# Optimization experiments

Measured on AMD Instinct MI355X. Metric: run time of the kernel, lower is better.

## Reference

```python
import jax, jax.numpy as jnp
import numpy as np
jax.config.update("jax_enable_x64", True)  # hashing uses int64 primes as in torch

N_PTS = 1048576
L, T, F = 16, 2 ** 18, 2
N_MIN, N_MAX = 16, 1024
HID, OUT = 64, 3


def setup_inputs() -> dict:
    key = jax.random.key(0)
    ks = jax.random.split(key, 6)
    X = jax.random.uniform(ks[0], (N_PTS, 2), dtype=jnp.float32)
    hash_table = jax.random.uniform(ks[1], (L, T, F), dtype=jnp.float32,
                                    minval=-1e-4, maxval=1e-4)
    def lin(k, fan_in, fan_out):
        bound = 1.0 / np.sqrt(fan_in)
        kw, kb = jax.random.split(k)
        W = jax.random.uniform(kw, (fan_in, fan_out), dtype=jnp.float32,
                               minval=-bound, maxval=bound)
        b = jax.random.uniform(kb, (fan_out,), dtype=jnp.float32,
                               minval=-bound, maxval=bound)
        return W, b
    W1, b1 = lin(ks[2], L * F, HID)
    W2, b2 = lin(ks[3], HID, HID)
    W3, b3 = lin(ks[4], HID, HID)
    W4, b4 = lin(ks[5], HID, OUT)
    return {"X": X, "hash_table": hash_table,
            "W1": W1, "b1": b1, "W2": W2, "b2": b2,
            "W3": W3, "b3": b3, "W4": W4, "b4": b4}


def reference(X, hash_table, W1, b1, W2, b2, W3, b3, W4, b4):
    Lh, Th, Fh = hash_table.shape
    # per-level resolutions: floor(N_min * b**l), b geometric between N_min and N_max
    b_geo = np.exp((np.log(N_MAX) - np.log(N_MIN)) / (Lh - 1))
    N_values = jnp.floor(jnp.asarray(N_MIN * b_geo ** np.arange(Lh),
                                     dtype=jnp.float32))  # (L,)

    x_scaled = X[:, :, None] * N_values[None, None, :]        # (N, 2, L)
    x_floor = jnp.floor(x_scaled)

    # NOTE: original code MULTIPLIES floor coords by the 0/1 vertex pattern
    # (not add) -- we replicate that math faithfully.
    vertices = jnp.array([[0., 0., 1., 1.], [0., 1., 0., 1.]],
                         dtype=jnp.float32)                   # (2, 4)
    x_vert = (x_floor[:, :, :, None] * vertices[None, :, None, :]
              ).astype(jnp.int64)                             # (N, 2, L, 4)

    primes = jnp.array([1, 2654435761], dtype=jnp.int64)
    hv = x_vert * primes[None, :, None, None]
    x_hash = jnp.remainder(jnp.bitwise_xor(hv[:, 0], hv[:, 1]), Th)  # (N, L, 4)

    # irregular gather: per-level hash table lookup -> (N, L, 4, F)
    lookup = hash_table[jnp.arange(Lh)[None, :, None], x_hash]

    w = x_scaled - x_floor                                    # (N, 2, L)
    fx, fy = w[:, 0, :], w[:, 1, :]
    cx, cy = 1.0 - fx, 1.0 - fy
    f_stack = jnp.stack([cx * cy, cx * fy, fx * cy, fx * fy], axis=2)  # (N, L, 4)

    x_interp = jnp.sum(f_stack[:, :, :, None] * lookup, axis=2)  # (N, L, F)
    feat = x_interp.reshape(-1, Lh * Fh).astype(jnp.float32)     # (N, 32)

    h = jax.nn.leaky_relu(feat @ W1 + b1)
    h = jax.nn.leaky_relu(h @ W2 + b2)
    h = jax.nn.leaky_relu(h @ W3 + b3)
    return jax.nn.relu(h @ W4 + b4)
```

## Files before the change

### kernel.cpp

```cpp
#include <hip/hip_runtime.h>
#include <math.h>

typedef _Float16 half8  __attribute__((ext_vector_type(8)));
typedef float    float4v __attribute__((ext_vector_type(4)));

constexpr int T_ = 1 << 18;
constexpr unsigned TMASK = T_ - 1;
constexpr unsigned PRIME = 2654435761u;

constexpr int WFRAG_HALFS = 22 * 64 * 8;
constexpr int BIAS_FLOATS = 208;
constexpr int WS_BYTES    = 22528 + 240 * 4;
constexpr int WS_UINT4    = WS_BYTES / 16;
constexpr int V12_OFF     = 23488;
constexpr int V3T_OFF     = 57344;
constexpr size_t V3T_BYTES = (size_t)16 * T_ * 4;

constexpr int BLK   = 256;
constexpr int PTS_PER_BLOCK = 512;

struct Meta { float n[16]; float off[16]; };

__global__ void prep_weights(const float* __restrict__ W1, const float* __restrict__ b1,
                             const float* __restrict__ W2, const float* __restrict__ b2,
                             const float* __restrict__ W3, const float* __restrict__ b3,
                             const float* __restrict__ W4, const float* __restrict__ b4,
                             const float2* __restrict__ table,
                             _Float16* __restrict__ wsW, float* __restrict__ wsB,
                             uint2* __restrict__ wsV, Meta mv)
{
    const int tid = threadIdx.x;
    const int bid = blockIdx.x;
    if (bid < 44) {
        const int e = bid * 256 + tid;
        const int frag = e >> 9;
        const int l    = (e >> 3) & 63;
        const int j    = e & 7;
        const int g = l >> 4, m = l & 15;
        const int u = j >> 2, r = j & 3;
        float v;
        if (frag < 4) {
            v = W1[(8*g + j) * 64 + 16*frag + m];
        } else if (frag < 12) {
            const int s = (frag - 4) >> 2, t = (frag - 4) & 3;
            v = W2[(32*s + 16*u + 4*g + r) * 64 + 16*t + m];
        } else if (frag < 20) {
            const int s = (frag - 12) >> 2, t = (frag - 12) & 3;
            v = W3[(32*s + 16*u + 4*g + r) * 64 + 16*t + m];
        } else {
            const int s = frag - 20;
            v = (m < 3) ? W4[(32*s + 16*u + 4*g + r) * 3 + m] : 0.f;
        }
        wsW[e] = (_Float16)v;
    } else if (bid == 44) {
        if (tid < 64) { wsB[tid] = b1[tid]; wsB[64 + tid] = b2[tid]; wsB[128 + tid] = b3[tid]; }
        else if (tid < 80)  { const int r2 = tid - 64; wsB[192 + r2] = (r2 < 3) ? b4[r2] : 0.f; }
        else if (tid < 96)  wsB[BIAS_FLOATS + (tid - 80)] = mv.n[tid - 80];
        else if (tid < 112) wsB[BIAS_FLOATS + 16 + (tid - 96)] = mv.off[tid - 96];
    } else {
        const int e = (bid - 45) * 256 + tid;
        const int total = (int)mv.off[15] + (int)mv.n[15] + 1;
        if (e < total) {
            int l = 0;
            #pragma unroll
            for (int k = 1; k < 16; ++k) if (e >= (int)mv.off[k]) l = k;
            const int i = e - (int)mv.off[l];
            const float2* tl = table + (size_t)l * T_;
            const float2 b = tl[((unsigned)i * PRIME) & TMASK];
            const float2 a = tl[i];
            union { _Float16 h[2]; unsigned u; } p0, p1;
            p0.h[0] = (_Float16)b.x; p0.h[1] = (_Float16)b.y;
            p1.h[0] = (_Float16)a.x; p1.h[1] = (_Float16)a.y;
            wsV[e] = uint2{p0.u, p1.u};
        }
    }
}

__global__ void prep_table_f16(const float2* __restrict__ table, unsigned* __restrict__ t16)
{
    const size_t i = (size_t)blockIdx.x * 256 + threadIdx.x;
    const float2 v = table[i];
    union { _Float16 h[2]; unsigned u; } p;
    p.h[0] = (_Float16)v.x; p.h[1] = (_Float16)v.y;
    t16[i] = p.u;
}

struct Gather {
    float2   v3f[4];
    unsigned v3u[4];
    unsigned v1[4];
    unsigned v2[4];
};

template<bool F16T>
__device__ __forceinline__ void issue_gather(Gather& G, const float2 xy,
                                             const float2* __restrict__ table,
                                             const unsigned* __restrict__ t16,
                                             const unsigned* __restrict__ gV12,
                                             const float (&nvq)[4], const int (&offq)[4],
                                             const int g)
{
    #pragma unroll
    for (int q = 0; q < 4; ++q) {
        const float n = nvq[q];
        const float xs = xy.x * n, ys = xy.y * n;
        const int xi = (int)floorf(xs);
        const int yi = (int)floorf(ys);
        const unsigned yp = (unsigned)yi * PRIME;
        const size_t idx = (size_t)(4*g + q) * T_ + (((unsigned)xi ^ yp) & TMASK);
        if constexpr (F16T) G.v3u[q] = t16[idx];
        else                G.v3f[q] = table[idx];
        G.v1[q] = gV12[2*(offq[q] + yi) + 0];
        G.v2[q] = gV12[2*(offq[q] + xi) + 1];
    }
}

template<bool F16T>
__device__ __forceinline__ half8 make_feat(const float2 xy, const Gather& G,
                                           const float (&nvq)[4],
                                           const float2 (&v0c)[4])
{
    half8 feat;
    #pragma unroll
    for (int q = 0; q < 4; ++q) {
        const float n = nvq[q];
        const float xs = xy.x * n, ys = xy.y * n;
        const float xf = floorf(xs), yf = floorf(ys);
        const float fx = xs - xf, fy = ys - yf;
        union { unsigned u; _Float16 h[2]; } u1, u2, u3;
        u1.u = G.v1[q]; u2.u = G.v2[q];
        float v3x, v3y;
        if constexpr (F16T) { u3.u = G.v3u[q]; v3x = (float)u3.h[0]; v3y = (float)u3.h[1]; }
        else                { v3x = G.v3f[q].x; v3y = G.v3f[q].y; }
        const float cx = 1.f - fx, cy = 1.f - fy;
        const float w0 = cx*cy, w1 = cx*fy, w2 = fx*cy, w3 = fx*fy;
        feat[2*q+0] = (_Float16)(w0*v0c[q].x + w1*(float)u1.h[0] + w2*(float)u2.h[0] + w3*v3x);
        feat[2*q+1] = (_Float16)(w0*v0c[q].y + w1*(float)u1.h[1] + w2*(float)u2.h[1] + w3*v3y);
    }
    return feat;
}

__device__ __forceinline__ void repack(const float4v (&acc)[4], half8& a0, half8& a1)
{
    #pragma unroll
    for (int u = 0; u < 2; ++u)
        #pragma unroll
        for (int r = 0; r < 4; ++r) {
            const float v0 = acc[u][r];
            const float v1 = acc[2 + u][r];
            a0[4*u + r] = (_Float16)(v0 > 0.f ? v0 : 0.01f * v0);
            a1[4*u + r] = (_Float16)(v1 > 0.f ? v1 : 0.01f * v1);
        }
}

template<bool F16T>
__global__ __launch_bounds__(BLK)
void fused_hashnerf_mfma(const float2* __restrict__ X,
                         const float2* __restrict__ table,
                         const uint4* __restrict__ ws,
                         float* __restrict__ out)
{
    __shared__ uint4 sRaw[WS_UINT4];

    const int tid = threadIdx.x;
    for (int i = tid; i < WS_UINT4; i += BLK) sRaw[i] = ws[i];
    __syncthreads();

    const _Float16* Wl = (const _Float16*)sRaw;
    const float*    Bl = (const float*)(sRaw + (22528 / 16));
    const unsigned* gV12 = (const unsigned*)((const char*)ws + V12_OFF);
    const unsigned* t16  = (const unsigned*)((const char*)ws + V3T_OFF);

    const int wave = tid >> 6, lane = tid & 63;
    const int g = lane >> 4, c = lane & 15;

    float4v b1f[4], b2f[4], b3f[4], b4f;
    #pragma unroll
    for (int t = 0; t < 4; ++t) {
        b1f[t] = *(const float4v*)(Bl +       16*t + 4*g);
        b2f[t] = *(const float4v*)(Bl +  64 + 16*t + 4*g);
        b3f[t] = *(const float4v*)(Bl + 128 + 16*t + 4*g);
    }
    b4f = *(const float4v*)(Bl + 192 + 4*g);
    float nvq[4];
    int   offq[4];
    #pragma unroll
    for (int q = 0; q < 4; ++q) {
        nvq[q]  = Bl[BIAS_FLOATS + 4*g + q];
        offq[q] = (int)Bl[BIAS_FLOATS + 16 + 4*g + q];
    }

    const int base_pt = blockIdx.x * PTS_PER_BLOCK + wave * 128;

    float2 xy[8];
    #pragma unroll
    for (int it = 0; it < 8; ++it) xy[it] = X[base_pt + it*16 + c];

    float2 v0c[4];
    #pragma unroll
    for (int q = 0; q < 4; ++q) v0c[q] = table[(size_t)(4*g + q) * T_];

    Gather G0, G1, G2;
    issue_gather<F16T>(G0, xy[0], table, t16, gV12, nvq, offq, g);
    issue_gather<F16T>(G1, xy[1], table, t16, gV12, nvq, offq, g);

    #pragma unroll
    for (int it = 0; it < 8; ++it) {
        Gather& Gc = (it % 3 == 0) ? G0 : (it % 3 == 1) ? G1 : G2;
        Gather& Gn = ((it + 2) % 3 == 0) ? G0 : ((it + 2) % 3 == 1) ? G1 : G2;

        const half8 feat = make_feat<F16T>(xy[it], Gc, nvq, v0c);

        if (it < 6) issue_gather<F16T>(Gn, xy[it+2], table, t16, gV12, nvq, offq, g);
        __builtin_amdgcn_sched_barrier(0);

        float4v acc[4];
        #pragma unroll
        for (int t = 0; t < 4; ++t) {
            const half8 wf = *(const half8*)(Wl + (t*64 + lane)*8);
            acc[t] = __builtin_amdgcn_mfma_f32_16x16x32_f16(wf, feat, b1f[t], 0, 0, 0);
        }

        half8 a0, a1;
        repack(acc, a0, a1);
        #pragma unroll
        for (int t = 0; t < 4; ++t) {
            const half8 w0f = *(const half8*)(Wl + ((4 + t)*64 + lane)*8);
            const half8 w1f = *(const half8*)(Wl + ((8 + t)*64 + lane)*8);
            float4v a = __builtin_amdgcn_mfma_f32_16x16x32_f16(w0f, a0, b2f[t], 0, 0, 0);
            acc[t]    = __builtin_amdgcn_mfma_f32_16x16x32_f16(w1f, a1, a,      0, 0, 0);
        }

        repack(acc, a0, a1);
        #pragma unroll
        for (int t = 0; t < 4; ++t) {
            const half8 w0f = *(const half8*)(Wl + ((12 + t)*64 + lane)*8);
            const half8 w1f = *(const half8*)(Wl + ((16 + t)*64 + lane)*8);
            float4v a = __builtin_amdgcn_mfma_f32_16x16x32_f16(w0f, a0, b3f[t], 0, 0, 0);
            acc[t]    = __builtin_amdgcn_mfma_f32_16x16x32_f16(w1f, a1, a,      0, 0, 0);
        }

        repack(acc, a0, a1);
        const half8 w40 = *(const half8*)(Wl + (20*64 + lane)*8);
        const half8 w41 = *(const half8*)(Wl + (21*64 + lane)*8);
        float4v o = __builtin_amdgcn_mfma_f32_16x16x32_f16(w40, a0, b4f, 0, 0, 0);
        o         = __builtin_amdgcn_mfma_f32_16x16x32_f16(w41, a1, o,   0, 0, 0);
        if (g == 0) {
            float* op = out + (size_t)3 * (base_pt + it * 16 + c);
            op[0] = fmaxf(o[0], 0.f);
            op[1] = fmaxf(o[1], 0.f);
            op[2] = fmaxf(o[2], 0.f);
        }
    }
}

extern "C" void kernel_launch(void* const* d_in, const int* in_sizes, int n_in,
                              void* d_out, int out_size, void* d_ws, size_t ws_size,
                              hipStream_t stream) {
    const float2* X     = (const float2*)d_in[0];
    const float2* table = (const float2*)d_in[1];
    const float*  W1    = (const float*)d_in[2];
    const float*  b1    = (const float*)d_in[3];
    const float*  W2    = (const float*)d_in[4];
    const float*  b2    = (const float*)d_in[5];
    const float*  W3    = (const float*)d_in[6];
    const float*  b3    = (const float*)d_in[7];
    const float*  W4    = (const float*)d_in[8];
    const float*  b4    = (const float*)d_in[9];
    float* out          = (float*)d_out;

    const int npts = in_sizes[0] / 2;

    Meta mv;
    const double bg = exp((log(1024.0) - log(16.0)) / 15.0);
    int acc = 0;
    for (int l = 0; l < 16; ++l) {
        const float nl = floorf((float)(16.0 * pow(bg, (double)l)));
        mv.n[l]   = nl;
        mv.off[l] = (float)acc;
        acc += (int)nl + 1;
    }

    _Float16* wsW = (_Float16*)d_ws;
    float*    wsB = (float*)((char*)d_ws + 22528);
    uint2*    wsV = (uint2*)((char*)d_ws + V12_OFF);
    unsigned* t16 = (unsigned*)((char*)d_ws + V3T_OFF);

    const bool f16t = ws_size >= (size_t)V3T_OFF + V3T_BYTES;

    prep_weights<<<62, 256, 0, stream>>>(W1, b1, W2, b2, W3, b3, W4, b4, table,
                                         wsW, wsB, wsV, mv);
    if (f16t) {
        prep_table_f16<<<16 * T_ / 256, 256, 0, stream>>>(table, t16);
        fused_hashnerf_mfma<true><<<npts / PTS_PER_BLOCK, BLK, 0, stream>>>(
            X, table, (const uint4*)d_ws, out);
    } else {
        fused_hashnerf_mfma<false><<<npts / PTS_PER_BLOCK, BLK, 0, stream>>>(
            X, table, (const uint4*)d_ws, out);
    }
}
```

Measured before the change: 213.4 us.

## Spatially bucket-sort input points before fused hash-grid MLP kernel

Adds a counting sort of input points into a 256x256 spatial grid (histogram, single-block scan, atomic scatter), then runs the fused kernel on the sorted points and writes outputs through the inverse permutation. The aim is better cache locality for the random hash-table gathers, since nearby points hit similar table entries. The cost is three extra kernels plus a memset and a large atomic histogram on every call. Output writes also become scattered, and the sorted path only runs when the workspace is large enough.

Measured after the change: 311.0 us. +45.8%, slower.

```diff
diff --git a/kernel.cpp b/kernel.cpp
--- a/kernel.cpp
+++ b/kernel.cpp
@@ -15,6 +15,8 @@
 constexpr int V12_OFF     = 23488;
 constexpr int V3T_OFF     = 57344;
 constexpr size_t V3T_BYTES = (size_t)16 * T_ * 4;
+constexpr size_t XS_OFF    = (size_t)V3T_OFF + V3T_BYTES;
+constexpr int NBUCK = 256 * 256;
 
 constexpr int BLK   = 256;
 constexpr int PTS_PER_BLOCK = 512;
@@ -85,6 +87,52 @@
     t16[i] = p.u;
 }
 
+__device__ __forceinline__ int bucket_key(const float2 p) {
+    int kx = (int)(p.x * 256.f); kx = kx > 255 ? 255 : kx;
+    int ky = (int)(p.y * 256.f); ky = ky > 255 ? 255 : ky;
+    return (ky << 8) | kx;
+}
+
+__global__ void s_hist(const float2* __restrict__ X, unsigned* __restrict__ hist, int npts)
+{
+    const int i = blockIdx.x * 256 + threadIdx.x;
+    if (i < npts) atomicAdd(&hist[bucket_key(X[i])], 1u);
+}
+
+__global__ __launch_bounds__(1024) void s_scan(unsigned* __restrict__ hist)
+{
+    __shared__ unsigned part[1024];
+    const int t = threadIdx.x;
+    unsigned sum = 0;
+    for (int k = 0; k < 64; ++k) sum += hist[t * 64 + k];
+    part[t] = sum;
+    __syncthreads();
+    for (int d = 1; d < 1024; d <<= 1) {
+        const unsigned v = (t >= d) ? part[t - d] : 0u;
+        __syncthreads();
+        part[t] += v;
+        __syncthreads();
+    }
+    unsigned run = (t == 0) ? 0u : part[t - 1];
+    for (int k = 0; k < 64; ++k) {
+        const unsigned c = hist[t * 64 + k];
+        hist[t * 64 + k] = run;
+        run += c;
+    }
+}
+
+__global__ void s_scatter(const float2* __restrict__ X, unsigned* __restrict__ off,
+                          float2* __restrict__ Xs, unsigned* __restrict__ idx, int npts)
+{
+    const int i = blockIdx.x * 256 + threadIdx.x;
+    if (i < npts) {
+        const float2 p = X[i];
+        const unsigned d = atomicAdd(&off[bucket_key(p)], 1u);
+        Xs[d] = p;
+        idx[d] = (unsigned)i;
+    }
+}
+
 struct Gather {
     float2   v3f[4];
     unsigned v3u[4];
@@ -92,7 +140,7 @@
     unsigned v2[4];
 };
 
-template<bool F16T>
+template<int MODE>
 __device__ __forceinline__ void issue_gather(Gather& G, const float2 xy,
                                              const float2* __restrict__ table,
                                              const unsigned* __restrict__ t16,
@@ -108,14 +156,14 @@
         const int yi = (int)floorf(ys);
         const unsigned yp = (unsigned)yi * PRIME;
         const size_t idx = (size_t)(4*g + q) * T_ + (((unsigned)xi ^ yp) & TMASK);
-        if constexpr (F16T) G.v3u[q] = t16[idx];
-        else                G.v3f[q] = table[idx];
+        if constexpr (MODE >= 1) G.v3u[q] = t16[idx];
+        else                     G.v3f[q] = table[idx];
         G.v1[q] = gV12[2*(offq[q] + yi) + 0];
         G.v2[q] = gV12[2*(offq[q] + xi) + 1];
     }
 }
 
-template<bool F16T>
+template<int MODE>
 __device__ __forceinline__ half8 make_feat(const float2 xy, const Gather& G,
                                            const float (&nvq)[4],
                                            const float2 (&v0c)[4])
@@ -130,8 +178,8 @@
         union { unsigned u; _Float16 h[2]; } u1, u2, u3;
         u1.u = G.v1[q]; u2.u = G.v2[q];
         float v3x, v3y;
-        if constexpr (F16T) { u3.u = G.v3u[q]; v3x = (float)u3.h[0]; v3y = (float)u3.h[1]; }
-        else                { v3x = G.v3f[q].x; v3y = G.v3f[q].y; }
+        if constexpr (MODE >= 1) { u3.u = G.v3u[q]; v3x = (float)u3.h[0]; v3y = (float)u3.h[1]; }
+        else                     { v3x = G.v3f[q].x; v3y = G.v3f[q].y; }
         const float cx = 1.f - fx, cy = 1.f - fy;
         const float w0 = cx*cy, w1 = cx*fy, w2 = fx*cy, w3 = fx*fy;
         feat[2*q+0] = (_Float16)(w0*v0c[q].x + w1*(float)u1.h[0] + w2*(float)u2.h[0] + w3*v3x);
@@ -153,11 +201,12 @@
         }
 }
 
-template<bool F16T>
+template<int MODE>
 __global__ __launch_bounds__(BLK)
 void fused_hashnerf_mfma(const float2* __restrict__ X,
                          const float2* __restrict__ table,
                          const uint4* __restrict__ ws,
+                         const unsigned* __restrict__ idx,
                          float* __restrict__ out)
 {
     __shared__ uint4 sRaw[WS_UINT4];
@@ -201,17 +250,17 @@
     for (int q = 0; q < 4; ++q) v0c[q] = table[(size_t)(4*g + q) * T_];
 
     Gather G0, G1, G2;
-    issue_gather<F16T>(G0, xy[0], table, t16, gV12, nvq, offq, g);
-    issue_gather<F16T>(G1, xy[1], table, t16, gV12, nvq, offq, g);
+    issue_gather<MODE>(G0, xy[0], table, t16, gV12, nvq, offq, g);
+    issue_gather<MODE>(G1, xy[1], table, t16, gV12, nvq, offq, g);
 
     #pragma unroll
     for (int it = 0; it < 8; ++it) {
         Gather& Gc = (it % 3 == 0) ? G0 : (it % 3 == 1) ? G1 : G2;
         Gather& Gn = ((it + 2) % 3 == 0) ? G0 : ((it + 2) % 3 == 1) ? G1 : G2;
 
-        const half8 feat = make_feat<F16T>(xy[it], Gc, nvq, v0c);
-
-        if (it < 6) issue_gather<F16T>(Gn, xy[it+2], table, t16, gV12, nvq, offq, g);
+        const half8 feat = make_feat<MODE>(xy[it], Gc, nvq, v0c);
+
+        if (it < 6) issue_gather<MODE>(Gn, xy[it+2], table, t16, gV12, nvq, offq, g);
         __builtin_amdgcn_sched_barrier(0);
 
         float4v acc[4];
@@ -246,7 +295,11 @@
         float4v o = __builtin_amdgcn_mfma_f32_16x16x32_f16(w40, a0, b4f, 0, 0, 0);
         o         = __builtin_amdgcn_mfma_f32_16x16x32_f16(w41, a1, o,   0, 0, 0);
         if (g == 0) {
-            float* op = out + (size_t)3 * (base_pt + it * 16 + c);
+            const int p = base_pt + it * 16 + c;
+            size_t oi;
+            if constexpr (MODE == 2) oi = idx[p];
+            else                     oi = (size_t)p;
+            float* op = out + 3 * oi;
             op[0] = fmaxf(o[0], 0.f);
             op[1] = fmaxf(o[1], 0.f);
             op[2] = fmaxf(o[2], 0.f);
@@ -286,16 +339,31 @@
     uint2*    wsV = (uint2*)((char*)d_ws + V12_OFF);
     unsigned* t16 = (unsigned*)((char*)d_ws + V3T_OFF);
 
-    const bool f16t = ws_size >= (size_t)V3T_OFF + V3T_BYTES;
+    const size_t idx_off  = XS_OFF + (size_t)npts * 8;
+    const size_t hist_off = idx_off + (size_t)npts * 4;
+    const size_t need_sorted = hist_off + (size_t)NBUCK * 4;
+
+    float2*   Xs   = (float2*)((char*)d_ws + XS_OFF);
+    unsigned* idx  = (unsigned*)((char*)d_ws + idx_off);
+    unsigned* hist = (unsigned*)((char*)d_ws + hist_off);
+
+    const int grid = npts / PTS_PER_BLOCK;
+    const int pblk = (npts + 255) / 256;
 
     prep_weights<<<62, 256, 0, stream>>>(W1, b1, W2, b2, W3, b3, W4, b4, table,
                                          wsW, wsB, wsV, mv);
-    if (f16t) {
+
+    if (ws_size >= need_sorted) {
         prep_table_f16<<<16 * T_ / 256, 256, 0, stream>>>(table, t16);
-        fused_hashnerf_mfma<true><<<npts / PTS_PER_BLOCK, BLK, 0, stream>>>(
-            X, table, (const uint4*)d_ws, out);
+        hipMemsetAsync(hist, 0, (size_t)NBUCK * 4, stream);
+        s_hist<<<pblk, 256, 0, stream>>>(X, hist, npts);
+        s_scan<<<1, 1024, 0, stream>>>(hist);
+        s_scatter<<<pblk, 256, 0, stream>>>(X, hist, Xs, idx, npts);
+        fused_hashnerf_mfma<2><<<grid, BLK, 0, stream>>>(Xs, table, (const uint4*)d_ws, idx, out);
+    } else if (ws_size >= (size_t)V3T_OFF + V3T_BYTES) {
+        prep_table_f16<<<16 * T_ / 256, 256, 0, stream>>>(table, t16);
+        fused_hashnerf_mfma<1><<<grid, BLK, 0, stream>>>(X, table, (const uint4*)d_ws, nullptr, out);
     } else {
-        fused_hashnerf_mfma<false><<<npts / PTS_PER_BLOCK, BLK, 0, stream>>>(
-            X, table, (const uint4*)d_ws, out);
-    }
-}
+        fused_hashnerf_mfma<0><<<grid, BLK, 0, stream>>>(X, table, (const uint4*)d_ws, nullptr, out);
+    }
+}
```
